# Performance work log

Measured on AMD Instinct MI355X. Metric: run time of the kernel, lower is better.

## Reference

```python
import jax, jax.numpy as jnp
import numpy as np

N_NODES = 8      # 4 regions + 4 boundaries
N_STEPS = 3


def _step_graph(nodes, Wd, Ws, b):
    """One all-pairs message-passing step.

    nodes: [N, B, C, H, W]
    Wd:    [N, C, C]  receiver-i conv weight acting on (nodes[j] - nodes[i])
    Ws:    [N, C, C]  receiver-i conv weight acting on nodes[i]
    b:     [N, C]
    edges[j][i] = Wd_i @ (nodes[j]-nodes[i]) + Ws_i @ nodes[i] + b_i   (1x1 conv)
    out[i] = sum_{j != i} relu(edges[j][i]) * nodes[j] + nodes[i]
    """
    # receiver-dependent self term: [N(i), B, C, H, W]
    self_term = jnp.einsum('iod,ibdhw->ibohw', Ws, nodes) + b[:, None, :, None, None]
    # pairwise differences nodes[j] - nodes[i]: [N(j), N(i), B, C, H, W]
    diff = nodes[:, None] - nodes[None, :]
    e = jnp.einsum('iod,jibdhw->jibohw', Wd, diff) + self_term[None]
    gate = jax.nn.relu(e)
    # zero out the diagonal (i == j contributes nothing)
    mask = (1.0 - jnp.eye(N_NODES, dtype=nodes.dtype))[:, :, None, None, None, None]
    gate = gate * mask
    # message[i] = sum_j gate[j,i] * nodes[j]
    msg = jnp.einsum('jibchw,jbchw->ibchw', gate, nodes)
    return msg + nodes


def setup_inputs() -> dict:
    key = jax.random.key(0)
    k1, k2, k3 = jax.random.split(key, 3)
    B, C, H, W = 4, 32, 96, 96
    nodes = jax.random.normal(k1, (N_NODES, B, C, H, W), dtype=jnp.float32)
    # 1x1 conv weights [N, C_out, 2C_in]; scaled ~1/(2C) to keep 3 steps numerically tame
    W_edge = jax.random.normal(k2, (N_NODES, C, 2 * C), dtype=jnp.float32) * 0.05
    b_edge = jax.random.normal(k3, (N_NODES, C), dtype=jnp.float32) * 0.05
    return {"nodes": nodes, "W_edge": W_edge, "b_edge": b_edge}


def reference(nodes, W_edge, b_edge):
    C = nodes.shape[2]
    Wd = W_edge[:, :, :C]   # acts on nodes[j] - nodes[i]
    Ws = W_edge[:, :, C:]   # acts on nodes[i]
    for _ in range(N_STEPS):
        nodes = _step_graph(nodes, Wd, Ws, b_edge)
    return nodes  # [N, B, C, H, W]; first half = regions, second half = boundaries
```

## Files before the change

kernel.cpp:

```cpp
#include <hip/hip_runtime.h>
#include <hip/hip_bf16.h>


#define NN 8
#define NSTEPS 3
#define BB 4
#define CC 32
#define HWSZ 9216
#define PX 16

typedef _Float16 f16x8 __attribute__((ext_vector_type(8)));
typedef _Float16 f16x4 __attribute__((ext_vector_type(4)));
typedef _Float16 f16x2 __attribute__((ext_vector_type(2)));
typedef float    f32x4 __attribute__((ext_vector_type(4)));
typedef float    f32x2 __attribute__((ext_vector_type(2)));

#define MFMA(A, B, C) __builtin_amdgcn_mfma_f32_16x16x32_f16((A), (B), (C), 0, 0, 0)

__device__ __forceinline__ void split2(float v, _Float16& h, _Float16& m) {
    h = (_Float16)v;
    m = (_Float16)(v - (float)h);
}

__global__ __launch_bounds__(64, 1)
void prep_w(const float* __restrict__ we, _Float16* __restrict__ wsf) {
    const int r    = blockIdx.x;
    const int lane = threadIdx.x;
    const int col  = lane & 15;
    const int quad = lane >> 4;
    #pragma unroll
    for (int t = 0; t < 2; ++t) {
        const float* wp = we + (size_t)((r * CC + 16 * t + col) * (2 * CC)) + quad * 8;
        f32x4 d0 = *(const f32x4*)wp;
        f32x4 d1 = *(const f32x4*)(wp + 4);
        f32x4 s0 = *(const f32x4*)(wp + CC);
        f32x4 s1 = *(const f32x4*)(wp + CC + 4);
        f16x8 dh, dm, sh, sm;
        #pragma unroll
        for (int k = 0; k < 8; ++k) {
            float d = (k < 4) ? d0[k & 3] : d1[k & 3];
            float s = (k < 4) ? s0[k & 3] : s1[k & 3];
            _Float16 h, m;
            split2(d, h, m);
            dh[k] = h; dm[k] = m;
            split2(s - d, h, m);
            sh[k] = h; sm[k] = m;
        }
        const int base = ((r * 2 + t) * 2) * 512 + lane * 8;
        *(f16x8*)&wsf[base]               = dh;
        *(f16x8*)&wsf[base + 512]         = dm;
        *(f16x8*)&wsf[16384 + base]       = sh;
        *(f16x8*)&wsf[16384 + base + 512] = sm;
    }
}

__global__ __launch_bounds__(512, 6)
void gcn3_f16w(const float* __restrict__ nodes,
               const _Float16* __restrict__ wsf,
               const float* __restrict__ be,
               float* __restrict__ out) {
    __shared__ _Float16 xsf[2][NN][64][8];
    __shared__ float    xgf[NN][2][64][4];

    const int tid  = threadIdx.x;
    const int wid  = tid >> 6;
    const int lane = tid & 63;
    const int col  = lane & 15;
    const int quad = lane >> 4;

    f16x8 awd[2][2];
    #pragma unroll
    for (int t = 0; t < 2; ++t)
        #pragma unroll
        for (int s = 0; s < 2; ++s)
            awd[t][s] = *(const f16x8*)&wsf[((wid * 2 + t) * 2 + s) * 512 + lane * 8];

    const int q0  = blockIdx.x * PX;
    const int b   = q0 / HWSZ;
    const int hw0 = q0 - b * HWSZ;

    #pragma unroll 1
    for (int kk = 0; kk < 2; ++kk) {
        int idx = tid + kk * 512;
        int p2 = (idx & 7) * 2;
        int c2 = ((idx >> 3) & 15) * 2;
        int n  = idx >> 7;
        const float* gp = nodes + (size_t)((n * BB + b) * CC + c2) * HWSZ + hw0 + p2;
        f32x2 v0 = *(const f32x2*)gp;
        f32x2 v1 = *(const f32x2*)(gp + HWSZ);
        #pragma unroll
        for (int e = 0; e < 2; ++e) {
            int px = p2 + e;
            _Float16 h0, m0, h1, m1;
            split2(v0[e], h0, m0);
            split2(v1[e], h1, m1);
            *(f16x2*)&xsf[0][n][(c2 >> 3) * 16 + px][c2 & 7] = f16x2{h0, h1};
            *(f16x2*)&xsf[1][n][(c2 >> 3) * 16 + px][c2 & 7] = f16x2{m0, m1};
            *(f32x2*)&xgf[n][c2 >> 4][((c2 >> 2) & 3) * 16 + px][c2 & 3] = f32x2{v0[e], v1[e]};
        }
    }
    __syncthreads();

    f32x4 msg[2];

    #pragma unroll 1
    for (int step = 0; step < NSTEPS; ++step) {
        f32x4 qf[2];
        {
            f16x8 bh = *(const f16x8*)&xsf[0][wid][lane][0];
            f16x8 bm = *(const f16x8*)&xsf[1][wid][lane][0];
            #pragma unroll
            for (int t = 0; t < 2; ++t) {
                f16x8 ah = *(const f16x8*)&wsf[16384 + ((wid * 2 + t) * 2 + 0) * 512 + lane * 8];
                f16x8 am = *(const f16x8*)&wsf[16384 + ((wid * 2 + t) * 2 + 1) * 512 + lane * 8];
                f32x4 q  = *(const f32x4*)&be[wid * CC + 16 * t + quad * 4];
                q = MFMA(am, bm, q);
                q = MFMA(am, bh, q);
                q = MFMA(ah, bm, q);
                qf[t] = MFMA(ah, bh, q);
            }
        }

        #pragma unroll
        for (int t = 0; t < 2; ++t)
            msg[t] = f32x4{0.f, 0.f, 0.f, 0.f};

        #pragma unroll
        for (int j = 0; j < NN; ++j) {
            if (j == wid) {
                #pragma unroll
                for (int t = 0; t < 2; ++t) {
                    f32x4 xgj = *(const f32x4*)&xgf[j][t][lane][0];
                    #pragma unroll
                    for (int k = 0; k < 4; ++k)
                        msg[t][k] += xgj[k];
                }
            } else {
                f16x8 bh = *(const f16x8*)&xsf[0][j][lane][0];
                f16x8 bm = *(const f16x8*)&xsf[1][j][lane][0];
                #pragma unroll
                for (int t = 0; t < 2; ++t) {
                    f32x4 xgj = *(const f32x4*)&xgf[j][t][lane][0];
                    f32x4 e = MFMA(awd[t][1], bh, qf[t]);
                    e = MFMA(awd[t][0], bm, e);
                    e = MFMA(awd[t][0], bh, e);
                    #pragma unroll
                    for (int k = 0; k < 4; ++k) {
                        float g = fmaxf(e[k], 0.f);
                        msg[t][k] = fmaf(g, xgj[k], msg[t][k]);
                    }
                }
            }
        }

        if (step < NSTEPS - 1) {
            __syncthreads();
            #pragma unroll
            for (int t = 0; t < 2; ++t) {
                f16x4 h4, m4;
                #pragma unroll
                for (int k = 0; k < 4; ++k) {
                    _Float16 h, m;
                    split2(msg[t][k], h, m);
                    h4[k] = h; m4[k] = m;
                }
                int lane2 = (2 * t + (quad >> 1)) * 16 + col;
                int e0    = (quad & 1) * 4;
                *(f16x4*)&xsf[0][wid][lane2][e0] = h4;
                *(f16x4*)&xsf[1][wid][lane2][e0] = m4;
                *(f32x4*)&xgf[wid][t][lane][0] = msg[t];
            }
            __syncthreads();
        }
    }

    #pragma unroll
    for (int t = 0; t < 2; ++t)
        #pragma unroll
        for (int k = 0; k < 4; ++k)
            out[(size_t)((wid * BB + b) * CC + 16 * t + quad * 4 + k) * HWSZ + hw0 + col] = msg[t][k];
}

extern "C" void kernel_launch(void* const* d_in, const int* in_sizes, int n_in,
                              void* d_out, int out_size, void* d_ws, size_t ws_size,
                              hipStream_t stream) {
    const float* nodes  = (const float*)d_in[0];
    const float* W_edge = (const float*)d_in[1];
    const float* b_edge = (const float*)d_in[2];
    float* outp = (float*)d_out;
    _Float16* wsf = (_Float16*)d_ws;

    prep_w<<<dim3(NN), dim3(64), 0, stream>>>(W_edge, wsf);

    dim3 grid((BB * HWSZ) / PX);
    dim3 block(512);
    gcn3_f16w<<<grid, block, 0, stream>>>(nodes, wsf, b_edge, outp);
}
```

Measured before the change: 136.9 us.

## Assign two receiver nodes per wave and share sender LDS loads

The block shrinks from 8 waves to 4, and each wave now handles two receiver nodes (w and w+4). Each sender's split-f16 operands and fp32 values are read from LDS once and used for both receivers, which halves LDS read traffic per MFMA. In exchange, each wave holds twice the weight and accumulator registers, and the launch bounds change to 256 threads with 4 blocks per CU.

```diff
diff --git a/kernel.cpp b/kernel.cpp
--- a/kernel.cpp
+++ b/kernel.cpp
@@ -8,6 +8,7 @@
 #define CC 32
 #define HWSZ 9216
 #define PX 16
+#define NR 2
 
 typedef _Float16 f16x8 __attribute__((ext_vector_type(8)));
 typedef _Float16 f16x4 __attribute__((ext_vector_type(4)));
@@ -54,7 +55,7 @@
     }
 }
 
-__global__ __launch_bounds__(512, 6)
+__global__ __launch_bounds__(256, 4)
 void gcn3_f16w(const float* __restrict__ nodes,
                const _Float16* __restrict__ wsf,
                const float* __restrict__ be,
@@ -63,25 +64,27 @@
     __shared__ float    xgf[NN][2][64][4];
 
     const int tid  = threadIdx.x;
-    const int wid  = tid >> 6;
+    const int w    = tid >> 6;
     const int lane = tid & 63;
     const int col  = lane & 15;
     const int quad = lane >> 4;
 
-    f16x8 awd[2][2];
+    f16x8 awd[NR][2][2];
     #pragma unroll
-    for (int t = 0; t < 2; ++t)
-        #pragma unroll
-        for (int s = 0; s < 2; ++s)
-            awd[t][s] = *(const f16x8*)&wsf[((wid * 2 + t) * 2 + s) * 512 + lane * 8];
+    for (int r = 0; r < NR; ++r)
+        #pragma unroll
+        for (int t = 0; t < 2; ++t)
+            #pragma unroll
+            for (int s = 0; s < 2; ++s)
+                awd[r][t][s] = *(const f16x8*)&wsf[(((w + 4 * r) * 2 + t) * 2 + s) * 512 + lane * 8];
 
     const int q0  = blockIdx.x * PX;
     const int b   = q0 / HWSZ;
     const int hw0 = q0 - b * HWSZ;
 
     #pragma unroll 1
-    for (int kk = 0; kk < 2; ++kk) {
-        int idx = tid + kk * 512;
+    for (int kk = 0; kk < 4; ++kk) {
+        int idx = tid + kk * 256;
         int p2 = (idx & 7) * 2;
         int c2 = ((idx >> 3) & 15) * 2;
         int n  = idx >> 7;
@@ -101,53 +104,60 @@
     }
     __syncthreads();
 
-    f32x4 msg[2];
+    f32x4 msg[NR][2];
 
     #pragma unroll 1
     for (int step = 0; step < NSTEPS; ++step) {
-        f32x4 qf[2];
-        {
-            f16x8 bh = *(const f16x8*)&xsf[0][wid][lane][0];
-            f16x8 bm = *(const f16x8*)&xsf[1][wid][lane][0];
+        f32x4 qf[NR][2];
+        #pragma unroll
+        for (int r = 0; r < NR; ++r) {
+            const int iw = w + 4 * r;
+            f16x8 bh = *(const f16x8*)&xsf[0][iw][lane][0];
+            f16x8 bm = *(const f16x8*)&xsf[1][iw][lane][0];
             #pragma unroll
             for (int t = 0; t < 2; ++t) {
-                f16x8 ah = *(const f16x8*)&wsf[16384 + ((wid * 2 + t) * 2 + 0) * 512 + lane * 8];
-                f16x8 am = *(const f16x8*)&wsf[16384 + ((wid * 2 + t) * 2 + 1) * 512 + lane * 8];
-                f32x4 q  = *(const f32x4*)&be[wid * CC + 16 * t + quad * 4];
+                f16x8 ah = *(const f16x8*)&wsf[16384 + ((iw * 2 + t) * 2 + 0) * 512 + lane * 8];
+                f16x8 am = *(const f16x8*)&wsf[16384 + ((iw * 2 + t) * 2 + 1) * 512 + lane * 8];
+                f32x4 q  = *(const f32x4*)&be[iw * CC + 16 * t + quad * 4];
                 q = MFMA(am, bm, q);
                 q = MFMA(am, bh, q);
                 q = MFMA(ah, bm, q);
-                qf[t] = MFMA(ah, bh, q);
+                qf[r][t] = MFMA(ah, bh, q);
             }
         }
 
         #pragma unroll
-        for (int t = 0; t < 2; ++t)
-            msg[t] = f32x4{0.f, 0.f, 0.f, 0.f};
+        for (int r = 0; r < NR; ++r)
+            #pragma unroll
+            for (int t = 0; t < 2; ++t)
+                msg[r][t] = f32x4{0.f, 0.f, 0.f, 0.f};
 
         #pragma unroll
         for (int j = 0; j < NN; ++j) {
-            if (j == wid) {
-                #pragma unroll
-                for (int t = 0; t < 2; ++t) {
-                    f32x4 xgj = *(const f32x4*)&xgf[j][t][lane][0];
-                    #pragma unroll
-                    for (int k = 0; k < 4; ++k)
-                        msg[t][k] += xgj[k];
-                }
-            } else {
-                f16x8 bh = *(const f16x8*)&xsf[0][j][lane][0];
-                f16x8 bm = *(const f16x8*)&xsf[1][j][lane][0];
-                #pragma unroll
-                for (int t = 0; t < 2; ++t) {
-                    f32x4 xgj = *(const f32x4*)&xgf[j][t][lane][0];
-                    f32x4 e = MFMA(awd[t][1], bh, qf[t]);
-                    e = MFMA(awd[t][0], bm, e);
-                    e = MFMA(awd[t][0], bh, e);
+            f16x8 bh = *(const f16x8*)&xsf[0][j][lane][0];
+            f16x8 bm = *(const f16x8*)&xsf[1][j][lane][0];
+            f32x4 xg0 = *(const f32x4*)&xgf[j][0][lane][0];
+            f32x4 xg1 = *(const f32x4*)&xgf[j][1][lane][0];
+            #pragma unroll
+            for (int r = 0; r < NR; ++r) {
+                if (j == w + 4 * r) {
                     #pragma unroll
                     for (int k = 0; k < 4; ++k) {
-                        float g = fmaxf(e[k], 0.f);
-                        msg[t][k] = fmaf(g, xgj[k], msg[t][k]);
+                        msg[r][0][k] += xg0[k];
+                        msg[r][1][k] += xg1[k];
+                    }
+                } else {
+                    #pragma unroll
+                    for (int t = 0; t < 2; ++t) {
+                        f32x4 e = MFMA(awd[r][t][1], bh, qf[r][t]);
+                        e = MFMA(awd[r][t][0], bm, e);
+                        e = MFMA(awd[r][t][0], bh, e);
+                        const f32x4& xg = (t == 0) ? xg0 : xg1;
+                        #pragma unroll
+                        for (int k = 0; k < 4; ++k) {
+                            float g = fmaxf(e[k], 0.f);
+                            msg[r][t][k] = fmaf(g, xg[k], msg[r][t][k]);
+                        }
                     }
                 }
             }
@@ -156,29 +166,35 @@
         if (step < NSTEPS - 1) {
             __syncthreads();
             #pragma unroll
-            for (int t = 0; t < 2; ++t) {
-                f16x4 h4, m4;
+            for (int r = 0; r < NR; ++r) {
+                const int iw = w + 4 * r;
                 #pragma unroll
-                for (int k = 0; k < 4; ++k) {
-                    _Float16 h, m;
-                    split2(msg[t][k], h, m);
-                    h4[k] = h; m4[k] = m;
+                for (int t = 0; t < 2; ++t) {
+                    f16x4 h4, m4;
+                    #pragma unroll
+                    for (int k = 0; k < 4; ++k) {
+                        _Float16 h, m;
+                        split2(msg[r][t][k], h, m);
+                        h4[k] = h; m4[k] = m;
+                    }
+                    int lane2 = (2 * t + (quad >> 1)) * 16 + col;
+                    int e0    = (quad & 1) * 4;
+                    *(f16x4*)&xsf[0][iw][lane2][e0] = h4;
+                    *(f16x4*)&xsf[1][iw][lane2][e0] = m4;
+                    *(f32x4*)&xgf[iw][t][lane][0] = msg[r][t];
                 }
-                int lane2 = (2 * t + (quad >> 1)) * 16 + col;
-                int e0    = (quad & 1) * 4;
-                *(f16x4*)&xsf[0][wid][lane2][e0] = h4;
-                *(f16x4*)&xsf[1][wid][lane2][e0] = m4;
-                *(f32x4*)&xgf[wid][t][lane][0] = msg[t];
             }
             __syncthreads();
         }
     }
 
     #pragma unroll
-    for (int t = 0; t < 2; ++t)
-        #pragma unroll
-        for (int k = 0; k < 4; ++k)
-            out[(size_t)((wid * BB + b) * CC + 16 * t + quad * 4 + k) * HWSZ + hw0 + col] = msg[t][k];
+    for (int r = 0; r < NR; ++r)
+        #pragma unroll
+        for (int t = 0; t < 2; ++t)
+            #pragma unroll
+            for (int k = 0; k < 4; ++k)
+                out[(size_t)(((w + 4 * r) * BB + b) * CC + 16 * t + quad * 4 + k) * HWSZ + hw0 + col] = msg[r][t][k];
 }
 
 extern "C" void kernel_launch(void* const* d_in, const int* in_sizes, int n_in,
@@ -193,6 +209,6 @@
     prep_w<<<dim3(NN), dim3(64), 0, stream>>>(W_edge, wsf);
 
     dim3 grid((BB * HWSZ) / PX);
-    dim3 block(512);
+    dim3 block(256);
     gcn3_f16w<<<grid, block, 0, stream>>>(nodes, wsf, b_edge, outp);
 }
```

Result: slower. 307.8 us (+124.8%).
